# Kernel tuning notes

Hardware: AMD Instinct MI355X
Metric: run time of the kernel (lower is better)

The kernel has to match this reference:

```python
import jax, jax.numpy as jnp
import numpy as np

B, S, V, H, O = 2048, 512, 32128, 16, 16


def setup_inputs() -> dict:
    key = jax.random.key(0)
    ks = jax.random.split(key, 7)
    x = jax.random.randint(ks[0], (B, S), 0, V)  # token ids
    enc1_w = jax.random.normal(ks[1], (H, V), dtype=jnp.float32) * 0.02
    enc1_b = jax.random.normal(ks[2], (H,), dtype=jnp.float32) * 0.02
    mean_w = jax.random.normal(ks[3], (O, H), dtype=jnp.float32) * 0.1
    mean_b = jax.random.normal(ks[4], (O,), dtype=jnp.float32) * 0.1
    logvar_w = jax.random.normal(ks[5], (O, H), dtype=jnp.float32) * 0.1
    logvar_b = jax.random.normal(ks[6], (O,), dtype=jnp.float32) * 0.1
    return {"x": x, "enc1_w": enc1_w, "enc1_b": enc1_b,
            "mean_w": mean_w, "mean_b": mean_b,
            "logvar_w": logvar_w, "logvar_b": logvar_b}


def reference(x, enc1_w, enc1_b, mean_w, mean_b, logvar_w, logvar_b):
    # one_hot(x, V).float().sum(1) == per-row token-count histogram [B, V]
    # (avoids materializing the [B, S, V] one-hot tensor)
    b, s = x.shape
    counts = jnp.zeros((b, V), dtype=jnp.float32).at[
        jnp.arange(b)[:, None], x].add(1.0)
    h = jax.nn.relu(counts @ enc1_w.T + enc1_b)  # [B, H]
    mean = h @ mean_w.T + mean_b                 # [B, O]
    logvar = h @ logvar_w.T + logvar_b           # [B, O]
    return (mean, logvar)
```

## Files before the change

kernel.cpp:

```cpp
#include <hip/hip_runtime.h>

#define B_ 2048
#define S_ 512
#define V_ 32128
#define H_ 16
#define O_ 16

__device__ __forceinline__ unsigned bf16rne(float f) {
    unsigned x = __float_as_uint(f);
    return (x + 0x7fffu + ((x >> 16) & 1u)) >> 16;
}

__global__ __launch_bounds__(256) void transpose_w_bf16_kernel(
    const float* __restrict__ w,
    unsigned* __restrict__ wT)
{
    __shared__ float tile[16][129];
    const int t  = threadIdx.x;
    const int v0 = blockIdx.x * 128;

#pragma unroll
    for (int i = 0; i < 8; ++i) {
        int idx = i * 256 + t;
        int h   = idx >> 7;
        int vl  = idx & 127;
        tile[h][vl] = w[(size_t)h * V_ + v0 + vl];
    }
    __syncthreads();
#pragma unroll
    for (int i = 0; i < 4; ++i) {
        int u  = i * 256 + t;
        int vl = u >> 3;
        int hw = u & 7;
        unsigned lo = bf16rne(tile[2 * hw][vl]);
        unsigned hi = bf16rne(tile[2 * hw + 1][vl]);
        wT[(size_t)(v0 + vl) * 8 + hw] = lo | (hi << 16);
    }
}

__global__ __launch_bounds__(256) void encoder_bf16_kernel(
    const int*   __restrict__ x,
    const uint4* __restrict__ wT,
    const float* __restrict__ enc1_b,
    const float* __restrict__ mean_w,
    const float* __restrict__ mean_b,
    const float* __restrict__ logvar_w,
    const float* __restrict__ logvar_b,
    float*       __restrict__ out)
{
    __shared__ int   toks[4][S_];
    __shared__ float hvec[4][16];

    const int t    = threadIdx.x;
    const int wave = t >> 6;
    const int lane = t & 63;
    const int b    = blockIdx.x * 4 + wave;

    {
        const int4* xr = (const int4*)(x + (size_t)b * S_);
        int4 t0 = xr[lane * 2];
        int4 t1 = xr[lane * 2 + 1];
        ((int4*)toks[wave])[lane * 2]     = t0;
        ((int4*)toks[wave])[lane * 2 + 1] = t1;
    }

    const int g = lane >> 1;
    const int p = lane & 1;

    float a[8];
#pragma unroll
    for (int k = 0; k < 8; ++k) a[k] = 0.0f;

#pragma unroll
    for (int j = 0; j < 16; ++j) {
        int v = toks[wave][j * 32 + g];
        uint4 wv = wT[(size_t)v * 2 + p];
        a[0] += __uint_as_float(wv.x << 16);
        a[1] += __uint_as_float(wv.x & 0xffff0000u);
        a[2] += __uint_as_float(wv.y << 16);
        a[3] += __uint_as_float(wv.y & 0xffff0000u);
        a[4] += __uint_as_float(wv.z << 16);
        a[5] += __uint_as_float(wv.z & 0xffff0000u);
        a[6] += __uint_as_float(wv.w << 16);
        a[7] += __uint_as_float(wv.w & 0xffff0000u);
    }

#pragma unroll
    for (int m = 2; m <= 32; m <<= 1) {
#pragma unroll
        for (int k = 0; k < 8; ++k) a[k] += __shfl_xor(a[k], m);
    }

    if (lane < 2) {
#pragma unroll
        for (int k = 0; k < 8; ++k) {
            float s = a[k] + enc1_b[p * 8 + k];
            hvec[wave][p * 8 + k] = fmaxf(s, 0.0f);
        }
    }

    if (lane < 32) {
        const int    o   = lane & 15;
        const int    sel = lane >> 4;
        const float* W   = sel ? logvar_w : mean_w;
        const float* Bv  = sel ? logvar_b : mean_b;
        float s = Bv[o];
#pragma unroll
        for (int k = 0; k < 16; ++k) s += W[o * 16 + k] * hvec[wave][k];
        out[(size_t)sel * B_ * O_ + (size_t)b * O_ + o] = s;
    }
}

__global__ __launch_bounds__(256) void encoder_f32_fallback_kernel(
    const int*   __restrict__ x,
    const float* __restrict__ table,
    const float* __restrict__ enc1_b,
    const float* __restrict__ mean_w,
    const float* __restrict__ mean_b,
    const float* __restrict__ logvar_w,
    const float* __restrict__ logvar_b,
    float*       __restrict__ out)
{
    __shared__ int   toks[S_];
    __shared__ float hred[4][16];
    __shared__ float hvec[16];

    const int t = threadIdx.x;
    const int b = blockIdx.x;
    {
        const int2* xr = (const int2*)(x + (size_t)b * S_);
        ((int2*)toks)[t] = xr[t];
    }
    __syncthreads();

    const int q = t & 3;
    const int g = t >> 2;
    float a0 = 0.f, a1 = 0.f, a2 = 0.f, a3 = 0.f;
#pragma unroll
    for (int j = 0; j < 8; ++j) {
        int v = toks[j * 64 + g];
        a0 += table[(size_t)(q * 4 + 0) * V_ + v];
        a1 += table[(size_t)(q * 4 + 1) * V_ + v];
        a2 += table[(size_t)(q * 4 + 2) * V_ + v];
        a3 += table[(size_t)(q * 4 + 3) * V_ + v];
    }
#pragma unroll
    for (int m = 4; m <= 32; m <<= 1) {
        a0 += __shfl_xor(a0, m);
        a1 += __shfl_xor(a1, m);
        a2 += __shfl_xor(a2, m);
        a3 += __shfl_xor(a3, m);
    }
    const int wave = t >> 6;
    const int lane = t & 63;
    if (lane < 4) {
        hred[wave][lane * 4 + 0] = a0;
        hred[wave][lane * 4 + 1] = a1;
        hred[wave][lane * 4 + 2] = a2;
        hred[wave][lane * 4 + 3] = a3;
    }
    __syncthreads();
    if (t < 16) {
        float s = hred[0][t] + hred[1][t] + hred[2][t] + hred[3][t] + enc1_b[t];
        hvec[t] = fmaxf(s, 0.0f);
    }
    __syncthreads();
    if (t < 32) {
        const int    o  = t & 15;
        const float* W  = (t < 16) ? mean_w : logvar_w;
        const float* Bv = (t < 16) ? mean_b : logvar_b;
        float s = Bv[o];
#pragma unroll
        for (int k = 0; k < 16; ++k) s += W[o * 16 + k] * hvec[k];
        const size_t off = (t < 16) ? 0 : (size_t)B_ * O_;
        out[off + (size_t)b * O_ + o] = s;
    }
}

extern "C" void kernel_launch(void* const* d_in, const int* in_sizes, int n_in,
                              void* d_out, int out_size, void* d_ws, size_t ws_size,
                              hipStream_t stream) {
    const int*   x        = (const int*)d_in[0];
    const float* enc1_w   = (const float*)d_in[1];
    const float* enc1_b   = (const float*)d_in[2];
    const float* mean_w   = (const float*)d_in[3];
    const float* mean_b   = (const float*)d_in[4];
    const float* logvar_w = (const float*)d_in[5];
    const float* logvar_b = (const float*)d_in[6];
    float*       out      = (float*)d_out;

    const size_t wT_bytes = (size_t)V_ * H_ * 2;
    if (ws_size >= wT_bytes) {
        unsigned* wT = (unsigned*)d_ws;
        transpose_w_bf16_kernel<<<V_ / 128, 256, 0, stream>>>(enc1_w, wT);
        encoder_bf16_kernel<<<B_ / 4, 256, 0, stream>>>(
            x, (const uint4*)wT, enc1_b, mean_w, mean_b, logvar_w, logvar_b, out);
    } else {
        encoder_f32_fallback_kernel<<<B_, 256, 0, stream>>>(
            x, enc1_w, enc1_b, mean_w, mean_b, logvar_w, logvar_b, out);
    }
}
```

Baseline: 17.88 us.

## Drop LDS staging in encoder and simplify weight transpose to direct per-column loads

Measured after the change: 16.94 us. 1.06x faster.

```diff
diff --git a/kernel.cpp b/kernel.cpp
--- a/kernel.cpp
+++ b/kernel.cpp
@@ -13,29 +13,22 @@
 
 __global__ __launch_bounds__(256) void transpose_w_bf16_kernel(
     const float* __restrict__ w,
-    unsigned* __restrict__ wT)
+    uint4* __restrict__ wT)
 {
-    __shared__ float tile[16][129];
-    const int t  = threadIdx.x;
-    const int v0 = blockIdx.x * 128;
-
-#pragma unroll
-    for (int i = 0; i < 8; ++i) {
-        int idx = i * 256 + t;
-        int h   = idx >> 7;
-        int vl  = idx & 127;
-        tile[h][vl] = w[(size_t)h * V_ + v0 + vl];
-    }
-    __syncthreads();
-#pragma unroll
-    for (int i = 0; i < 4; ++i) {
-        int u  = i * 256 + t;
-        int vl = u >> 3;
-        int hw = u & 7;
-        unsigned lo = bf16rne(tile[2 * hw][vl]);
-        unsigned hi = bf16rne(tile[2 * hw + 1][vl]);
-        wT[(size_t)(v0 + vl) * 8 + hw] = lo | (hi << 16);
-    }
+    const int col = blockIdx.x * 256 + threadIdx.x;
+    if (col >= V_) return;
+
+    float r[16];
+#pragma unroll
+    for (int h = 0; h < 16; ++h) r[h] = w[(size_t)h * V_ + col];
+
+    unsigned u[8];
+#pragma unroll
+    for (int k = 0; k < 8; ++k)
+        u[k] = bf16rne(r[2 * k]) | (bf16rne(r[2 * k + 1]) << 16);
+
+    wT[(size_t)col * 2 + 0] = make_uint4(u[0], u[1], u[2], u[3]);
+    wT[(size_t)col * 2 + 1] = make_uint4(u[4], u[5], u[6], u[7]);
 }
 
 __global__ __launch_bounds__(256) void encoder_bf16_kernel(
@@ -48,33 +41,37 @@
     const float* __restrict__ logvar_b,
     float*       __restrict__ out)
 {
-    __shared__ int   toks[4][S_];
-    __shared__ float hvec[4][16];
-
     const int t    = threadIdx.x;
     const int wave = t >> 6;
     const int lane = t & 63;
     const int b    = blockIdx.x * 4 + wave;
 
-    {
-        const int4* xr = (const int4*)(x + (size_t)b * S_);
-        int4 t0 = xr[lane * 2];
-        int4 t1 = xr[lane * 2 + 1];
-        ((int4*)toks[wave])[lane * 2]     = t0;
-        ((int4*)toks[wave])[lane * 2 + 1] = t1;
-    }
-
     const int g = lane >> 1;
     const int p = lane & 1;
 
+    const int    o   = lane & 15;
+    const int    sel = (lane >> 4) & 1;
+    const float* Wrow = (sel ? logvar_w : mean_w) + o * 16;
+    float4 w0 = ((const float4*)Wrow)[0];
+    float4 w1 = ((const float4*)Wrow)[1];
+    float4 w2 = ((const float4*)Wrow)[2];
+    float4 w3 = ((const float4*)Wrow)[3];
+    float  bv = (sel ? logvar_b : mean_b)[o];
+    float4 eb = ((const float4*)enc1_b)[p * 2 + 0];
+    float4 eb2 = ((const float4*)enc1_b)[p * 2 + 1];
+
+    const int* xr = x + (size_t)b * S_;
+    int v[16];
+#pragma unroll
+    for (int j = 0; j < 16; ++j)
+        v[j] = __builtin_nontemporal_load(xr + j * 32 + g);
+
     float a[8];
 #pragma unroll
     for (int k = 0; k < 8; ++k) a[k] = 0.0f;
-
 #pragma unroll
     for (int j = 0; j < 16; ++j) {
-        int v = toks[wave][j * 32 + g];
-        uint4 wv = wT[(size_t)v * 2 + p];
+        uint4 wv = wT[(size_t)v[j] * 2 + p];
         a[0] += __uint_as_float(wv.x << 16);
         a[1] += __uint_as_float(wv.x & 0xffff0000u);
         a[2] += __uint_as_float(wv.y << 16);
@@ -91,23 +88,30 @@
         for (int k = 0; k < 8; ++k) a[k] += __shfl_xor(a[k], m);
     }
 
-    if (lane < 2) {
-#pragma unroll
-        for (int k = 0; k < 8; ++k) {
-            float s = a[k] + enc1_b[p * 8 + k];
-            hvec[wave][p * 8 + k] = fmaxf(s, 0.0f);
-        }
+    const float ebv[8] = {eb.x, eb.y, eb.z, eb.w, eb2.x, eb2.y, eb2.z, eb2.w};
+    float hs[8];
+#pragma unroll
+    for (int k = 0; k < 8; ++k) hs[k] = fmaxf(a[k] + ebv[k], 0.0f);
+
+    float ho[8];
+#pragma unroll
+    for (int k = 0; k < 8; ++k) ho[k] = __shfl_xor(hs[k], 1);
+
+    float hv[16];
+#pragma unroll
+    for (int k = 0; k < 8; ++k) {
+        hv[k]     = p ? ho[k] : hs[k];
+        hv[8 + k] = p ? hs[k] : ho[k];
     }
 
     if (lane < 32) {
-        const int    o   = lane & 15;
-        const int    sel = lane >> 4;
-        const float* W   = sel ? logvar_w : mean_w;
-        const float* Bv  = sel ? logvar_b : mean_b;
-        float s = Bv[o];
-#pragma unroll
-        for (int k = 0; k < 16; ++k) s += W[o * 16 + k] * hvec[wave][k];
-        out[(size_t)sel * B_ * O_ + (size_t)b * O_ + o] = s;
+        float s = bv;
+        s += w0.x * hv[0]  + w0.y * hv[1]  + w0.z * hv[2]  + w0.w * hv[3];
+        s += w1.x * hv[4]  + w1.y * hv[5]  + w1.z * hv[6]  + w1.w * hv[7];
+        s += w2.x * hv[8]  + w2.y * hv[9]  + w2.z * hv[10] + w2.w * hv[11];
+        s += w3.x * hv[12] + w3.y * hv[13] + w3.z * hv[14] + w3.w * hv[15];
+        __builtin_nontemporal_store(
+            s, out + (size_t)sel * B_ * O_ + (size_t)b * O_ + o);
     }
 }
 
@@ -191,10 +195,10 @@
 
     const size_t wT_bytes = (size_t)V_ * H_ * 2;
     if (ws_size >= wT_bytes) {
-        unsigned* wT = (unsigned*)d_ws;
-        transpose_w_bf16_kernel<<<V_ / 128, 256, 0, stream>>>(enc1_w, wT);
+        uint4* wT = (uint4*)d_ws;
+        transpose_w_bf16_kernel<<<(V_ + 255) / 256, 256, 0, stream>>>(enc1_w, wT);
         encoder_bf16_kernel<<<B_ / 4, 256, 0, stream>>>(
-            x, (const uint4*)wT, enc1_b, mean_w, mean_b, logvar_w, logvar_b, out);
+            x, wT, enc1_b, mean_w, mean_b, logvar_w, logvar_b, out);
     } else {
         encoder_f32_fallback_kernel<<<B_, 256, 0, stream>>>(
             x, enc1_w, enc1_b, mean_w, mean_b, logvar_w, logvar_b, out);
```
